# Kernel tuning notes

Hardware: AMD Instinct MI355X
Metric: run time of the kernel (lower is better)

The kernel has to match this reference:

```python
import jax, jax.numpy as jnp
import numpy as np

H = 256    # hidden_size
CVQ = 64   # vq_ph_channel
K = 128    # vq_ph_codebook_dim
NL = 5     # num_layers per ConvBlocks
NB = 2     # layers_in_block
KS = 3     # kernel_size


def _ln_c(x, g, b, eps=1e-5):
    # LayerNorm over channel dim of a [B, C, T] tensor
    m = jnp.mean(x, axis=1, keepdims=True)
    v = jnp.mean((x - m) ** 2, axis=1, keepdims=True)
    return (x - m) * jax.lax.rsqrt(v + eps) * g[None, :, None] + b[None, :, None]


def _causal_conv(x, w, b):
    # x [B,Cin,T], w [Cout,Cin,K]; left (causal) padding of K-1
    y = jax.lax.conv_general_dilated(x, w, (1,), [(w.shape[-1] - 1, 0)],
                                     dimension_numbers=('NCH', 'OIH', 'NCH'))
    return y + b[None, :, None]


def _pw(x, w, b):
    # pointwise (kernel-size-1) conv: w [Cout, Cin]
    return jnp.einsum('oi,bit->bot', w, x) + b[None, :, None]


def _conv_blocks(x, mask, ln_g, ln_b, w1, b1, w2, b2, last_g, last_b, post_w, post_b):
    # LeftPadConvBlocks: NL residual blocks x NB sub-blocks of
    # LN -> causal conv (C->2C, k=3) -> *k^-0.5 -> GELU -> 1x1 conv (2C->C), residual + mask
    scale = KS ** -0.5
    for i in range(NL):
        for j in range(NB):
            h = _ln_c(x, ln_g[i, j], ln_b[i, j])
            h = _causal_conv(h, w1[i, j], b1[i, j]) * scale
            h = jax.nn.gelu(h, approximate=False)
            h = _pw(h, w2[i, j], b2[i, j])
            x = (x + h) * mask
    x = _ln_c(x, last_g, last_b) * mask
    x = _causal_conv(x, post_w, post_b) * mask
    return x


def _group_by_segs(h_bct, mel2ph, L):
    # scatter-mean mel frames into phoneme segments; index 0 = padding (dropped)
    h = jnp.swapaxes(h_bct, 1, 2)  # [B, T, H]
    def one(hb, mb):
        s = jnp.zeros((L + 1, hb.shape[-1]), hb.dtype).at[mb].add(hb)
        c = jnp.zeros((L + 1,), hb.dtype).at[mb].add(1.0)
        return s[1:] / jnp.clip(c[1:], 1.0)[:, None]
    g = jax.vmap(one)(h, mel2ph)   # [B, L, H]
    return jnp.swapaxes(g, 1, 2)   # [B, H, L]


def _vq(z, codebook, beta=0.25):
    # EMA-VQ forward math: nearest-codebook lookup + straight-through + commitment loss
    x = jnp.swapaxes(z, 1, 2)                                # [B, T, C]
    d = (jnp.sum(x ** 2, -1, keepdims=True)
         - 2.0 * jnp.einsum('btc,kc->btk', x, codebook)
         + jnp.sum(codebook ** 2, -1))                       # [B, T, K]
    idx = jnp.argmin(d, axis=-1)                             # [B, T]
    q = codebook[idx]                                        # [B, T, C]
    loss = beta * jnp.mean((x - jax.lax.stop_gradient(q)) ** 2)
    q_st = x + jax.lax.stop_gradient(q - x)
    return jnp.swapaxes(q_st, 1, 2), loss, idx


def setup_inputs() -> dict:
    key = jax.random.key(0)
    ks = list(jax.random.split(key, 64))
    it = iter(ks)
    B, T, L = 16, 2048, 512
    f = lambda shape, s: jax.random.normal(next(it), shape, jnp.float32) * s
    inp = {}
    inp['x'] = jax.random.normal(next(it), (B, 80, T), jnp.float32)
    inp['in_nonpadding'] = jnp.ones((B, 1, T), jnp.float32)
    inp['in_mel2ph'] = jnp.sort(jax.random.randint(next(it), (B, T), 1, L + 1), axis=-1)
    inp['ph_nonpadding'] = jnp.ones((B, 1, L), jnp.float32)
    inp['conv_in_w'] = f((H, 80), 0.05)
    inp['conv_in_b'] = jnp.zeros((H,), jnp.float32)
    for p in ('enc', 'pn'):
        inp[p + '_ln_g'] = jnp.ones((NL, NB, H), jnp.float32)
        inp[p + '_ln_b'] = jnp.zeros((NL, NB, H), jnp.float32)
        inp[p + '_w1'] = f((NL, NB, 2 * H, H, KS), 0.03)
        inp[p + '_b1'] = jnp.zeros((NL, NB, 2 * H), jnp.float32)
        inp[p + '_w2'] = f((NL, NB, H, 2 * H), 0.03)
        inp[p + '_b2'] = jnp.zeros((NL, NB, H), jnp.float32)
        inp[p + '_last_g'] = jnp.ones((H,), jnp.float32)
        inp[p + '_last_b'] = jnp.zeros((H,), jnp.float32)
        inp[p + '_post_w'] = f((H, H, KS), 0.03)
        inp[p + '_post_b'] = jnp.zeros((H,), jnp.float32)
    inp['proj_in_w'] = f((CVQ, H), 0.05)
    inp['proj_in_b'] = jnp.zeros((CVQ,), jnp.float32)
    inp['proj_out_w'] = f((H, CVQ), 0.05)
    inp['proj_out_b'] = jnp.zeros((H,), jnp.float32)
    inp['codebook'] = f((K, CVQ), 0.1)
    return inp


def reference(x, in_nonpadding, in_mel2ph, ph_nonpadding,
              conv_in_w, conv_in_b,
              enc_ln_g, enc_ln_b, enc_w1, enc_b1, enc_w2, enc_b2,
              enc_last_g, enc_last_b, enc_post_w, enc_post_b,
              pn_ln_g, pn_ln_b, pn_w1, pn_b1, pn_w2, pn_b2,
              pn_last_g, pn_last_b, pn_post_w, pn_post_b,
              proj_in_w, proj_in_b, proj_out_w, proj_out_b, codebook):
    L = ph_nonpadding.shape[-1]
    h = _pw(x, conv_in_w, conv_in_b) * in_nonpadding                     # ph_conv_in
    h = _conv_blocks(h, in_nonpadding, enc_ln_g, enc_ln_b, enc_w1, enc_b1,
                     enc_w2, enc_b2, enc_last_g, enc_last_b,
                     enc_post_w, enc_post_b) * in_nonpadding             # ph_encoder
    h = _group_by_segs(h, in_mel2ph, L)                                  # [B, H, L]
    h = _conv_blocks(h, ph_nonpadding, pn_ln_g, pn_ln_b, pn_w1, pn_b1,
                     pn_w2, pn_b2, pn_last_g, pn_last_b,
                     pn_post_w, pn_post_b) * ph_nonpadding               # ph_postnet
    z = _pw(h, proj_in_w, proj_in_b)                                     # ph_latents_proj_in
    q, vq_loss, idx = _vq(z, codebook)                                   # VQ
    out = _pw(q, proj_out_w, proj_out_b)                                 # ph_latents_proj_out
    return out, vq_loss, idx
```

## Files before the change

kernel.cpp:

```cpp
#include <hip/hip_runtime.h>
#include <hip/hip_bf16.h>


typedef unsigned short u16;
typedef unsigned int u32;
typedef __attribute__((ext_vector_type(8))) _Float16 f16x8;
typedef __attribute__((ext_vector_type(16))) float f32x16;

#define OUT_LOSS_OFF 2097152
#define OUT_IDX_OFF  2097153

__device__ __forceinline__ void split_f16(float x, u16& h, u16& l) {
    union { _Float16 f; u16 u; } a, b;
    a.f = (_Float16)x;
    float hf = (float)a.f;
    b.f = (_Float16)(x - hf);
    h = a.u; l = b.u;
}

__device__ __forceinline__ void gelu_pack(float v, float bb, u16* GH, u16* GL,
                                          int off) {
    const float ks = 0.5773502691896258f;
    float y = (v + bb) * ks;
    float ge = 0.5f * y * (1.0f + erff(y * 0.7071067811865476f));
    u16 h, l; split_f16(ge, h, l);
    GH[off] = h; GL[off] = l;
}

__global__ __launch_bounds__(256) void k_t_mat(const float* __restrict__ w,
                                               float* __restrict__ wt,
                                               int G, int O, int I) {
    size_t n = (size_t)G * O * I;
    for (size_t i = (size_t)blockIdx.x * 256 + threadIdx.x; i < n;
         i += (size_t)gridDim.x * 256) {
        int ci = (int)(i % I);
        int o  = (int)((i / I) % O);
        int g  = (int)(i / ((size_t)I * O));
        wt[((size_t)g * I + ci) * O + o] = w[i];
    }
}

__global__ __launch_bounds__(256) void k_t_w1mf(const float* __restrict__ w,
                                                u16* __restrict__ BH,
                                                u16* __restrict__ BL, int S) {
    size_t N = (size_t)S * 3 * 16 * 16 * 64 * 8;
    for (size_t i = (size_t)blockIdx.x * 256 + threadIdx.x; i < N;
         i += (size_t)gridDim.x * 256) {
        int j = (int)(i & 7); size_t r = i >> 3;
        int L = (int)(r & 63); r >>= 6;
        int nt = (int)(r & 15); r >>= 4;
        int kb = (int)(r & 15); r >>= 4;
        int k3 = (int)(r % 3); int s = (int)(r / 3);
        int oc = nt * 32 + (L & 31);
        int c = kb * 16 + ((L >> 5) << 3) + j;
        float v = w[(((size_t)s * 512 + oc) * 256 + c) * 3 + k3];
        u16 h, l; split_f16(v, h, l);
        BH[i] = h; BL[i] = l;
    }
}

__global__ __launch_bounds__(256) void k_t_w2mf(const float* __restrict__ w,
                                                u16* __restrict__ BH,
                                                u16* __restrict__ BL, int S) {
    size_t N = (size_t)S * 32 * 8 * 64 * 8;
    for (size_t i = (size_t)blockIdx.x * 256 + threadIdx.x; i < N;
         i += (size_t)gridDim.x * 256) {
        int j = (int)(i & 7);
        int L = (int)((i >> 3) & 63);
        int nt = (int)((i >> 9) & 7);
        int kb = (int)((i >> 12) & 31);
        int s = (int)(i >> 17);
        int oc = nt * 32 + (L & 31);
        int ic = kb * 16 + ((L >> 5) << 3) + j;
        float v = w[((size_t)s * 256 + oc) * 512 + ic];
        u16 h, l; split_f16(v, h, l);
        BH[i] = h; BL[i] = l;
    }
}

__global__ __launch_bounds__(256) void k_t_wpmf(const float* __restrict__ w,
                                                u16* __restrict__ BH,
                                                u16* __restrict__ BL) {
    int i = blockIdx.x * 256 + threadIdx.x;
    int j = i & 7;
    int L = (i >> 3) & 63;
    int nt = (i >> 9) & 7;
    int kb = (i >> 12) & 15;
    int k3 = i >> 16;
    int oc = nt * 32 + (L & 31);
    int c = kb * 16 + ((L >> 5) << 3) + j;
    float v = w[((size_t)oc * 256 + c) * 3 + k3];
    u16 h, l; split_f16(v, h, l);
    BH[i] = h; BL[i] = l;
}

template <int CIN, int COUT, int CHUNK, bool STATS>
__global__ __launch_bounds__(256) void k_pw(const float* __restrict__ x,
                                            const float* __restrict__ wt,
                                            const float* __restrict__ bias,
                                            const float* __restrict__ mask,
                                            float* __restrict__ y,
                                            float* __restrict__ MM,
                                            float* __restrict__ IV, int T) {
    extern __shared__ float X[];
    constexpr int NG = COUT / CHUNK;
    __shared__ float rs[64 * NG], rs2[64 * NG];
    const int b = blockIdx.y, t0 = blockIdx.x * 64;
    for (int i = threadIdx.x; i < CIN * 64; i += 256) {
        int ci = i >> 6, j = i & 63;
        X[i] = x[((size_t)b * CIN + ci) * T + t0 + j];
    }
    __syncthreads();
    const int tl = threadIdx.x & 63;
    const int g = __builtin_amdgcn_readfirstlane((int)(threadIdx.x >> 6));
    float acc[CHUNK];
#pragma unroll
    for (int o = 0; o < CHUNK; o++) acc[o] = 0.f;
    for (int i = 0; i < CIN; i++) {
        float xv = X[i * 64 + tl];
        const float* wr = wt + (size_t)i * COUT + g * CHUNK;
#pragma unroll
        for (int o = 0; o < CHUNK; o++) acc[o] = fmaf(wr[o], xv, acc[o]);
    }
    float mk = mask ? mask[(size_t)b * T + t0 + tl] : 1.0f;
    float s = 0.f, s2 = 0.f;
#pragma unroll
    for (int o = 0; o < CHUNK; o++) {
        int oc = g * CHUNK + o;
        float val = (acc[o] + bias[oc]) * mk;
        y[((size_t)b * COUT + oc) * T + t0 + tl] = val;
        s += val; s2 += val * val;
    }
    if constexpr (STATS) {
        rs[g * 64 + tl] = s; rs2[g * 64 + tl] = s2;
        __syncthreads();
        if (threadIdx.x < 64) {
            float ss = 0.f, ss2 = 0.f;
#pragma unroll
            for (int gg = 0; gg < NG; gg++) {
                ss += rs[gg * 64 + threadIdx.x];
                ss2 += rs2[gg * 64 + threadIdx.x];
            }
            float m = ss * (1.0f / COUT);
            float var = ss2 * (1.0f / COUT) - m * m;
            MM[(size_t)b * T + t0 + threadIdx.x] = m;
            IV[(size_t)b * T + t0 + threadIdx.x] = 1.0f / sqrtf(var + 1e-5f);
        }
    }
}

template <int M>
__global__ __launch_bounds__(512, 4) void k_sub(
    const float* __restrict__ xin, float* __restrict__ xout,
    const float* __restrict__ MMi, const float* __restrict__ IVi,
    const float* __restrict__ lng, const float* __restrict__ lnb,
    const u16* __restrict__ B1H, const u16* __restrict__ B1L,
    const float* __restrict__ b1,
    const u16* __restrict__ B2H, const u16* __restrict__ B2L,
    const float* __restrict__ b2, const float* __restrict__ mask,
    float* __restrict__ MMo, float* __restrict__ IVo, int T) {
    constexpr int MT = M / 32;
    constexpr int SH = (M + 2) * 264 * 2;
    constexpr int CG = 512 / M;
    constexpr int CPT = 256 / CG;
    __shared__ __align__(16) char smem[2 * SH + 4096];
    u16* LH = (u16*)smem;
    u16* LL = (u16*)(smem + SH);
    u16* GH = (u16*)smem;
    u16* GL = (u16*)(smem + SH);
    float* SOUT = (float*)smem;
    float* rs  = (float*)(smem + 2 * SH);
    float* rs2 = (float*)(smem + 2 * SH + 2048);

    const int tid = threadIdx.x;
    const int b = blockIdx.y, t0 = blockIdx.x * M;
    const size_t xoff = (size_t)b * 256 * T;
    const size_t bT = (size_t)b * T;

    {
        int jj = tid & (M - 1);
        int cg = tid / M;
        int t = t0 - 2 + jj;
        bool ok = (t >= 0);
        float m = ok ? MMi[bT + t] : 0.f;
        float v = ok ? IVi[bT + t] : 0.f;
#pragma unroll
        for (int i = 0; i < CPT; i++) {
            int c = cg + i * CG;
            float xv = ok ? xin[xoff + (size_t)c * T + t] : 0.f;
            float ln = ok ? ((xv - m) * v * lng[c] + lnb[c]) : 0.f;
            u16 h, l; split_f16(ln, h, l);
            LH[jj * 264 + c] = h; LL[jj * 264 + c] = l;
        }
        int j2 = M + (tid >> 8);
        int c2 = tid & 255;
        int t2 = t0 + (M - 2) + (tid >> 8);
        float m2 = MMi[bT + t2], v2 = IVi[bT + t2];
        float x2 = xin[xoff + (size_t)c2 * T + t2];
        float ln2 = (x2 - m2) * v2 * lng[c2] + lnb[c2];
        u16 h2, l2; split_f16(ln2, h2, l2);
        LH[j2 * 264 + c2] = h2; LL[j2 * 264 + c2] = l2;
    }
    __syncthreads();

    const int lane = tid & 63;
    const int w = tid >> 6;
    const int arow = lane & 31;
    const int acol = (lane >> 5) << 3;
    const int thalf = (lane >> 5) << 2;
    const int oc_l = w * 32 + (lane & 31);
    const u16* b1h0 = B1H + (size_t)w * 512 + (size_t)lane * 8;
    const u16* b1l0 = B1L + (size_t)w * 512 + (size_t)lane * 8;
    const u16* b1h1 = B1H + (size_t)(8 + w) * 512 + (size_t)lane * 8;
    const u16* b1l1 = B1L + (size_t)(8 + w) * 512 + (size_t)lane * 8;
    const u16* b2h = B2H + (size_t)w * 512 + (size_t)lane * 8;
    const u16* b2l = B2L + (size_t)w * 512 + (size_t)lane * 8;

    f32x16 c0[MT], c1[MT];
#pragma unroll
    for (int m = 0; m < MT; m++)
#pragma unroll
        for (int r = 0; r < 16; r++) { c0[m][r] = 0.f; c1[m][r] = 0.f; }
    __builtin_amdgcn_s_setprio(1);
#pragma unroll 2
    for (int kk = 0; kk < 48; kk++) {
        int k3 = kk >> 4, kb = kk & 15;
        f16x8 bh0 = *(const f16x8*)(b1h0 + (size_t)kk * 8192);
        f16x8 bl0 = *(const f16x8*)(b1l0 + (size_t)kk * 8192);
        f16x8 bh1 = *(const f16x8*)(b1h1 + (size_t)kk * 8192);
        f16x8 bl1 = *(const f16x8*)(b1l1 + (size_t)kk * 8192);
#pragma unroll
        for (int m = 0; m < MT; m++) {
            int ao = (m * 32 + arow + k3) * 264 + kb * 16 + acol;
            f16x8 ah = *(const f16x8*)&LH[ao];
            f16x8 al = *(const f16x8*)&LL[ao];
            c0[m] = __builtin_amdgcn_mfma_f32_32x32x16_f16(ah, bh0, c0[m], 0, 0, 0);
            c1[m] = __builtin_amdgcn_mfma_f32_32x32x16_f16(ah, bh1, c1[m], 0, 0, 0);
            c0[m] = __builtin_amdgcn_mfma_f32_32x32x16_f16(ah, bl0, c0[m], 0, 0, 0);
            c1[m] = __builtin_amdgcn_mfma_f32_32x32x16_f16(ah, bl1, c1[m], 0, 0, 0);
            c0[m] = __builtin_amdgcn_mfma_f32_32x32x16_f16(al, bh0, c0[m], 0, 0, 0);
            c1[m] = __builtin_amdgcn_mfma_f32_32x32x16_f16(al, bh1, c1[m], 0, 0, 0);
        }
    }
    __builtin_amdgcn_s_setprio(0);
    __syncthreads();

    {
        float bb = b1[oc_l];
#pragma unroll
        for (int m = 0; m < MT; m++)
#pragma unroll
            for (int r = 0; r < 16; r++) {
                int trow = m * 32 + thalf + ((r >> 2) << 3) + (r & 3);
                gelu_pack(c0[m][r], bb, GH, GL, trow * 264 + oc_l);
            }
    }
    __syncthreads();

#pragma unroll
    for (int m = 0; m < MT; m++)
#pragma unroll
        for (int r = 0; r < 16; r++) c0[m][r] = 0.f;
    __builtin_amdgcn_s_setprio(1);
#pragma unroll 2
    for (int i = 0; i < 16; i++) {
        f16x8 bh2 = *(const f16x8*)(b2h + (size_t)i * 4096);
        f16x8 bl2 = *(const f16x8*)(b2l + (size_t)i * 4096);
#pragma unroll
        for (int m = 0; m < MT; m++) {
            int go = (m * 32 + arow) * 264 + i * 16 + acol;
            f16x8 gh = *(const f16x8*)&GH[go];
            f16x8 gl = *(const f16x8*)&GL[go];
            c0[m] = __builtin_amdgcn_mfma_f32_32x32x16_f16(gh, bh2, c0[m], 0, 0, 0);
            c0[m] = __builtin_amdgcn_mfma_f32_32x32x16_f16(gh, bl2, c0[m], 0, 0, 0);
            c0[m] = __builtin_amdgcn_mfma_f32_32x32x16_f16(gl, bh2, c0[m], 0, 0, 0);
        }
    }
    __builtin_amdgcn_s_setprio(0);
    __syncthreads();

    {
        float bb = b1[256 + oc_l];
#pragma unroll
        for (int m = 0; m < MT; m++)
#pragma unroll
            for (int r = 0; r < 16; r++) {
                int trow = m * 32 + thalf + ((r >> 2) << 3) + (r & 3);
                gelu_pack(c1[m][r], bb, GH, GL, trow * 264 + oc_l);
            }
    }
    __syncthreads();

    __builtin_amdgcn_s_setprio(1);
#pragma unroll 2
    for (int i = 0; i < 16; i++) {
        f16x8 bh2 = *(const f16x8*)(b2h + (size_t)(16 + i) * 4096);
        f16x8 bl2 = *(const f16x8*)(b2l + (size_t)(16 + i) * 4096);
#pragma unroll
        for (int m = 0; m < MT; m++) {
            int go = (m * 32 + arow) * 264 + i * 16 + acol;
            f16x8 gh = *(const f16x8*)&GH[go];
            f16x8 gl = *(const f16x8*)&GL[go];
            c0[m] = __builtin_amdgcn_mfma_f32_32x32x16_f16(gh, bh2, c0[m], 0, 0, 0);
            c0[m] = __builtin_amdgcn_mfma_f32_32x32x16_f16(gh, bl2, c0[m], 0, 0, 0);
            c0[m] = __builtin_amdgcn_mfma_f32_32x32x16_f16(gl, bh2, c0[m], 0, 0, 0);
        }
    }
    __builtin_amdgcn_s_setprio(0);
    __syncthreads();

#pragma unroll
    for (int m = 0; m < MT; m++)
#pragma unroll
        for (int r = 0; r < 16; r++) {
            int trow = m * 32 + thalf + ((r >> 2) << 3) + (r & 3);
            SOUT[trow * 260 + oc_l] = c0[m][r];
        }
    __syncthreads();
    {
        int t = tid & (M - 1), cg = tid / M;
        float mk = mask[bT + t0 + t];
        float s = 0.f, s2 = 0.f;
#pragma unroll
        for (int i = 0; i < CPT; i++) {
            int c = cg * CPT + i;
            size_t adr = xoff + (size_t)c * T + t0 + t;
            float val = (xin[adr] + SOUT[t * 260 + c] + b2[c]) * mk;
            xout[adr] = val;
            s += val; s2 += val * val;
        }
        rs[tid] = s; rs2[tid] = s2;
    }
    __syncthreads();
    if (tid < M) {
        float ss = 0.f, ss2 = 0.f;
#pragma unroll
        for (int k = 0; k < CG; k++) {
            ss += rs[k * M + tid]; ss2 += rs2[k * M + tid];
        }
        float m = ss * (1.0f / 256.0f);
        float var = ss2 * (1.0f / 256.0f) - m * m;
        MMo[bT + t0 + tid] = m;
        IVo[bT + t0 + tid] = 1.0f / sqrtf(var + 1e-5f);
    }
}

__global__ __launch_bounds__(1024, 4) void k_sub16(
    const float* __restrict__ xin, float* __restrict__ xout,
    const float* __restrict__ MMi, const float* __restrict__ IVi,
    const float* __restrict__ lng, const float* __restrict__ lnb,
    const u16* __restrict__ B1H, const u16* __restrict__ B1L,
    const float* __restrict__ b1,
    const u16* __restrict__ B2H, const u16* __restrict__ B2L,
    const float* __restrict__ b2, const float* __restrict__ mask,
    float* __restrict__ MMo, float* __restrict__ IVo, int T) {
    __shared__ __align__(16) char smem[76800];
    u16* LH = (u16*)smem;
    u16* LL = (u16*)(smem + 17952);
    u16* GH = (u16*)smem;
    u16* GL = (u16*)(smem + 34304);
    float* SOUT = (float*)smem;
    float* rs  = (float*)(smem + 68608);
    float* rs2 = (float*)(smem + 72704);

    const int tid = threadIdx.x;
    const int b = blockIdx.y, t0 = blockIdx.x * 32;
    const size_t xoff = (size_t)b * 256 * T;
    const size_t bT = (size_t)b * T;

    {
        int jj = tid & 31;
        int cg = tid >> 5;
        int t = t0 - 2 + jj;
        bool ok = (t >= 0);
        float m = ok ? MMi[bT + t] : 0.f;
        float v = ok ? IVi[bT + t] : 0.f;
#pragma unroll
        for (int i = 0; i < 8; i++) {
            int c = cg + i * 32;
            float xv = ok ? xin[xoff + (size_t)c * T + t] : 0.f;
            float ln = ok ? ((xv - m) * v * lng[c] + lnb[c]) : 0.f;
            u16 h, l; split_f16(ln, h, l);
            LH[jj * 264 + c] = h; LL[jj * 264 + c] = l;
        }
        if (tid < 512) {
            int j2 = 32 + (tid >> 8);
            int c2 = tid & 255;
            int t2 = t0 + 30 + (tid >> 8);
            float ln2 = (xin[xoff + (size_t)c2 * T + t2] - MMi[bT + t2]) *
                        IVi[bT + t2] * lng[c2] + lnb[c2];
            u16 h2, l2; split_f16(ln2, h2, l2);
            LH[j2 * 264 + c2] = h2; LL[j2 * 264 + c2] = l2;
        }
    }
    __syncthreads();

    const int lane = tid & 63;
    const int w = tid >> 6;
    const int arow = lane & 31;
    const int acol = (lane >> 5) << 3;
    const int thalf = (lane >> 5) << 2;
    const int oc_l = w * 32 + (lane & 31);
    const u16* b1h = B1H + (size_t)w * 512 + (size_t)lane * 8;
    const u16* b1l = B1L + (size_t)w * 512 + (size_t)lane * 8;

    f32x16 cc;
#pragma unroll
    for (int r = 0; r < 16; r++) cc[r] = 0.f;
    __builtin_amdgcn_s_setprio(1);
#pragma unroll 4
    for (int kk = 0; kk < 48; kk++) {
        int k3 = kk >> 4, kb = kk & 15;
        int ao = (arow + k3) * 264 + kb * 16 + acol;
        f16x8 ah = *(const f16x8*)&LH[ao];
        f16x8 al = *(const f16x8*)&LL[ao];
        f16x8 bh = *(const f16x8*)(b1h + (size_t)kk * 8192);
        f16x8 bl = *(const f16x8*)(b1l + (size_t)kk * 8192);
        cc = __builtin_amdgcn_mfma_f32_32x32x16_f16(ah, bh, cc, 0, 0, 0);
        cc = __builtin_amdgcn_mfma_f32_32x32x16_f16(ah, bl, cc, 0, 0, 0);
        cc = __builtin_amdgcn_mfma_f32_32x32x16_f16(al, bh, cc, 0, 0, 0);
    }
    __builtin_amdgcn_s_setprio(0);
    __syncthreads();

    {
        float bb = b1[oc_l];
#pragma unroll
        for (int r = 0; r < 16; r++) {
            int trow = thalf + ((r >> 2) << 3) + (r & 3);
            gelu_pack(cc[r], bb, GH, GL, trow * 536 + oc_l);
        }
    }
    __syncthreads();

    const int nt2 = w & 7;
    const int ih = w >> 3;
    const u16* b2h = B2H + (size_t)nt2 * 512 + (size_t)lane * 8;
    const u16* b2l = B2L + (size_t)nt2 * 512 + (size_t)lane * 8;
#pragma unroll
    for (int r = 0; r < 16; r++) cc[r] = 0.f;
    __builtin_amdgcn_s_setprio(1);
#pragma unroll 4
    for (int i = 0; i < 16; i++) {
        int ii = ih * 16 + i;
        int go = arow * 536 + ii * 16 + acol;
        f16x8 gh = *(const f16x8*)&GH[go];
        f16x8 gl = *(const f16x8*)&GL[go];
        f16x8 bh2 = *(const f16x8*)(b2h + (size_t)ii * 4096);
        f16x8 bl2 = *(const f16x8*)(b2l + (size_t)ii * 4096);
        cc = __builtin_amdgcn_mfma_f32_32x32x16_f16(gh, bh2, cc, 0, 0, 0);
        cc = __builtin_amdgcn_mfma_f32_32x32x16_f16(gh, bl2, cc, 0, 0, 0);
        cc = __builtin_amdgcn_mfma_f32_32x32x16_f16(gl, bh2, cc, 0, 0, 0);
    }
    __builtin_amdgcn_s_setprio(0);
    __syncthreads();

    if (w < 8) {
#pragma unroll
        for (int r = 0; r < 16; r++) {
            int trow = thalf + ((r >> 2) << 3) + (r & 3);
            SOUT[trow * 260 + oc_l] = cc[r];
        }
    }
    __syncthreads();
    if (w >= 8) {
        int oc2 = nt2 * 32 + (lane & 31);
#pragma unroll
        for (int r = 0; r < 16; r++) {
            int trow = thalf + ((r >> 2) << 3) + (r & 3);
            SOUT[trow * 260 + oc2] += cc[r];
        }
    }
    __syncthreads();
    {
        int t = tid & 31, cg = tid >> 5;
        float mk = mask[bT + t0 + t];
        float s = 0.f, s2 = 0.f;
#pragma unroll
        for (int i = 0; i < 8; i++) {
            int c = cg * 8 + i;
            size_t adr = xoff + (size_t)c * T + t0 + t;
            float val = (xin[adr] + SOUT[t * 260 + c] + b2[c]) * mk;
            xout[adr] = val;
            s += val; s2 += val * val;
        }
        rs[tid] = s; rs2[tid] = s2;
    }
    __syncthreads();
    if (tid < 32) {
        float ss = 0.f, ss2 = 0.f;
#pragma unroll
        for (int k = 0; k < 32; k++) {
            ss += rs[k * 32 + tid]; ss2 += rs2[k * 32 + tid];
        }
        float m = ss * (1.0f / 256.0f);
        float var = ss2 * (1.0f / 256.0f) - m * m;
        MMo[bT + t0 + tid] = m;
        IVo[bT + t0 + tid] = 1.0f / sqrtf(var + 1e-5f);
    }
}

template <int M>
__global__ __launch_bounds__(512, (M == 32 ? 8 : 4)) void k_lnc(
    const float* __restrict__ xin, float* __restrict__ xout,
    const float* __restrict__ MM, const float* __restrict__ IV,
    const float* __restrict__ lg, const float* __restrict__ lb,
    const u16* __restrict__ BH, const u16* __restrict__ BL,
    const float* __restrict__ bias, const float* __restrict__ mask, int T) {
    constexpr int MT = M / 32;
    constexpr int SH = (M + 2) * 264 * 2;
    constexpr int CG = 512 / M;
    constexpr int CPT = 256 / CG;
    __shared__ __align__(16) char smem[2 * SH];
    u16* LH = (u16*)smem;
    u16* LL = (u16*)(smem + SH);
    float* SOUT = (float*)smem;

    const int tid = threadIdx.x;
    const int b = blockIdx.y, t0 = blockIdx.x * M;
    const size_t xoff = (size_t)b * 256 * T;
    const size_t bT = (size_t)b * T;

    {
        int jj = tid & (M - 1);
        int cg = tid / M;
        int t = t0 - 2 + jj;
        bool ok = (t >= 0);
        float m = ok ? MM[bT + t] : 0.f;
        float v = ok ? IV[bT + t] : 0.f;
        float mk = ok ? mask[bT + t] : 0.f;
#pragma unroll
        for (int i = 0; i < CPT; i++) {
            int c = cg + i * CG;
            float xv = ok ? xin[xoff + (size_t)c * T + t] : 0.f;
            float ln = ok ? ((xv - m) * v * lg[c] + lb[c]) * mk : 0.f;
            u16 h, l; split_f16(ln, h, l);
            LH[jj * 264 + c] = h; LL[jj * 264 + c] = l;
        }
        int j2 = M + (tid >> 8);
        int c2 = tid & 255;
        int t2 = t0 + (M - 2) + (tid >> 8);
        float ln2 = ((xin[xoff + (size_t)c2 * T + t2] - MM[bT + t2]) *
                     IV[bT + t2] * lg[c2] + lb[c2]) * mask[bT + t2];
        u16 h2, l2; split_f16(ln2, h2, l2);
        LH[j2 * 264 + c2] = h2; LL[j2 * 264 + c2] = l2;
    }
    __syncthreads();

    const int lane = tid & 63;
    const int w = tid >> 6;
    const int arow = lane & 31;
    const int acol = (lane >> 5) << 3;
    const int thalf = (lane >> 5) << 2;
    const u16* bph = BH + (size_t)w * 512 + (size_t)lane * 8;
    const u16* bpl = BL + (size_t)w * 512 + (size_t)lane * 8;

    f32x16 aH[MT], aM[MT];
#pragma unroll
    for (int m = 0; m < MT; m++)
#pragma unroll
        for (int r = 0; r < 16; r++) { aH[m][r] = 0.f; aM[m][r] = 0.f; }
    __builtin_amdgcn_s_setprio(1);
#pragma unroll 2
    for (int kk = 0; kk < 48; kk++) {
        int k3 = kk >> 4, kb = kk & 15;
        f16x8 bh = *(const f16x8*)(bph + (size_t)kk * 4096);
        f16x8 bl = *(const f16x8*)(bpl + (size_t)kk * 4096);
#pragma unroll
        for (int m = 0; m < MT; m++) {
            int ao = (m * 32 + arow + k3) * 264 + kb * 16 + acol;
            f16x8 ah = *(const f16x8*)&LH[ao];
            f16x8 al = *(const f16x8*)&LL[ao];
            aH[m] = __builtin_amdgcn_mfma_f32_32x32x16_f16(ah, bh, aH[m], 0, 0, 0);
            aM[m] = __builtin_amdgcn_mfma_f32_32x32x16_f16(ah, bl, aM[m], 0, 0, 0);
            aM[m] = __builtin_amdgcn_mfma_f32_32x32x16_f16(al, bh, aM[m], 0, 0, 0);
        }
    }
    __builtin_amdgcn_s_setprio(0);
    __syncthreads();
    {
        int oc = w * 32 + (lane & 31);
#pragma unroll
        for (int m = 0; m < MT; m++)
#pragma unroll
            for (int r = 0; r < 16; r++) {
                int trow = m * 32 + thalf + ((r >> 2) << 3) + (r & 3);
                SOUT[trow * 260 + oc] = aH[m][r] + aM[m][r];
            }
    }
    __syncthreads();
    {
        int t = tid & (M - 1), cg = tid / M;
        float mk = mask[bT + t0 + t];
#pragma unroll
        for (int i = 0; i < CPT; i++) {
            int c = cg * CPT + i;
            xout[xoff + (size_t)c * T + t0 + t] =
                (SOUT[t * 260 + c] + bias[c]) * mk;
        }
    }
}

__global__ __launch_bounds__(256) void k_counts(const int* __restrict__ m2p,
                                                int* __restrict__ cnt) {
    __shared__ int c[512];
    int b = blockIdx.x;
    for (int i = threadIdx.x; i < 512; i += 256) c[i] = 0;
    __syncthreads();
    for (int t = threadIdx.x; t < 2048; t += 256) {
        int p = m2p[b * 2048 + t];
        if (p >= 1 && p <= 512) atomicAdd(&c[p - 1], 1);
    }
    __syncthreads();
    for (int i = threadIdx.x; i < 512; i += 256) cnt[b * 512 + i] = c[i];
}

__global__ __launch_bounds__(256) void k_scatter(const float* __restrict__ h,
                                                 const int* __restrict__ m2p,
                                                 float* __restrict__ g) {
    extern __shared__ float sm[];
    float* HT = sm;
    int* ph = (int*)(sm + 256 * 65);
    int b = blockIdx.y, t0 = blockIdx.x * 64;
    if (threadIdx.x < 64) ph[threadIdx.x] = m2p[b * 2048 + t0 + threadIdx.x];
    for (int i = threadIdx.x; i < 256 * 64; i += 256) {
        int c = i >> 6, j = i & 63;
        HT[c * 65 + j] = h[((size_t)b * 256 + c) * 2048 + t0 + j];
    }
    __syncthreads();
    int c = threadIdx.x;
    float run = 0.f;
    int cur = ph[0];
    for (int j = 0; j < 64; j++) {
        int p = ph[j];
        if (p != cur) {
            if (cur >= 1 && cur <= 512)
                atomicAdd(&g[((size_t)b * 256 + c) * 512 + cur - 1], run);
            run = 0.f;
            cur = p;
        }
        run += HT[c * 65 + j];
    }
    if (cur >= 1 && cur <= 512)
        atomicAdd(&g[((size_t)b * 256 + c) * 512 + cur - 1], run);
}

__global__ __launch_bounds__(512) void k_postprep(float* __restrict__ g,
                                                  const int* __restrict__ cnt,
                                                  float* __restrict__ MM,
                                                  float* __restrict__ IV) {
    int b = blockIdx.x, l = threadIdx.x;
    int c1 = cnt[b * 512 + l];
    if (c1 < 1) c1 = 1;
    float rc = 1.0f / (float)c1;
    float s = 0.f, s2 = 0.f;
    for (int c = 0; c < 256; c++) {
        size_t idx = ((size_t)b * 256 + c) * 512 + l;
        float v = g[idx] * rc;
        g[idx] = v;
        s += v; s2 += v * v;
    }
    float m = s * (1.0f / 256.0f);
    float var = s2 * (1.0f / 256.0f) - m * m;
    MM[(size_t)b * 512 + l] = m;
    IV[(size_t)b * 512 + l] = 1.0f / sqrtf(var + 1e-5f);
}

__global__ __launch_bounds__(256) void k_vq(const float* __restrict__ z,
                                            const float* __restrict__ cb,
                                            int* __restrict__ idxout,
                                            float* __restrict__ out,
                                            float* __restrict__ lossacc) {
    int n = blockIdx.x * 256 + threadIdx.x;
    int b = n >> 9, l = n & 511;
    float zr[64];
#pragma unroll
    for (int c = 0; c < 64; c++) zr[c] = z[((size_t)b * 64 + c) * 512 + l];
    float best = 3.4e38f;
    int bi = 0;
    for (int k = 0; k < 128; k++) {
        const float* cr = cb + k * 64;
        float d = 0.f;
#pragma unroll
        for (int c = 0; c < 64; c++) {
            float t = zr[c] - cr[c];
            d = fmaf(t, t, d);
        }
        if (d < best) { best = d; bi = k; }
    }
    idxout[n] = bi;
    out[OUT_IDX_OFF + n] = (float)bi;
    atomicAdd(lossacc, best);
}

__global__ void k_loss(const float* __restrict__ acc, float* __restrict__ out) {
    if (threadIdx.x == 0 && blockIdx.x == 0)
        out[OUT_LOSS_OFF] = 0.25f * acc[0] * (1.0f / 524288.0f);
}

__global__ __launch_bounds__(256) void k_projout(const float* __restrict__ cb,
                                                 const int* __restrict__ idx,
                                                 const float* __restrict__ wt,
                                                 const float* __restrict__ bias,
                                                 float* __restrict__ out) {
    __shared__ float Q[64 * 64];
    __shared__ int ids[64];
    int b = blockIdx.y, l0 = blockIdx.x * 64;
    if (threadIdx.x < 64) ids[threadIdx.x] = idx[b * 512 + l0 + threadIdx.x];
    __syncthreads();
    for (int i = threadIdx.x; i < 4096; i += 256) {
        int c = i >> 6, l = i & 63;
        Q[c * 64 + l] = cb[ids[l] * 64 + c];
    }
    __syncthreads();
    int tl = threadIdx.x & 63;
    int g = __builtin_amdgcn_readfirstlane((int)(threadIdx.x >> 6));
    float acc[64];
#pragma unroll
    for (int o = 0; o < 64; o++) acc[o] = 0.f;
    for (int i = 0; i < 64; i++) {
        float xv = Q[i * 64 + tl];
        const float* wr = wt + i * 256 + g * 64;
#pragma unroll
        for (int o = 0; o < 64; o++) acc[o] = fmaf(wr[o], xv, acc[o]);
    }
#pragma unroll
    for (int o = 0; o < 64; o++) {
        int oc = g * 64 + o;
        out[(size_t)b * 131072 + (size_t)oc * 512 + l0 + tl] = acc[o] + bias[oc];
    }
}

extern "C" void kernel_launch(void* const* d_in, const int* in_sizes, int n_in,
                              void* d_out, int out_size, void* d_ws, size_t ws_size,
                              hipStream_t stream) {
    (void)in_sizes; (void)n_in; (void)out_size; (void)ws_size;
    const float* x          = (const float*)d_in[0];
    const float* in_np      = (const float*)d_in[1];
    const int*   mel2ph     = (const int*)d_in[2];
    const float* ph_np      = (const float*)d_in[3];
    const float* conv_in_w  = (const float*)d_in[4];
    const float* conv_in_b  = (const float*)d_in[5];
    const float* e_ln_g = (const float*)d_in[6];
    const float* e_ln_b = (const float*)d_in[7];
    const float* e_w1   = (const float*)d_in[8];
    const float* e_b1   = (const float*)d_in[9];
    const float* e_w2   = (const float*)d_in[10];
    const float* e_b2   = (const float*)d_in[11];
    const float* e_lg   = (const float*)d_in[12];
    const float* e_lb   = (const float*)d_in[13];
    const float* e_pw   = (const float*)d_in[14];
    const float* e_pb   = (const float*)d_in[15];
    const float* p_ln_g = (const float*)d_in[16];
    const float* p_ln_b = (const float*)d_in[17];
    const float* p_w1   = (const float*)d_in[18];
    const float* p_b1   = (const float*)d_in[19];
    const float* p_w2   = (const float*)d_in[20];
    const float* p_b2   = (const float*)d_in[21];
    const float* p_lg   = (const float*)d_in[22];
    const float* p_lb   = (const float*)d_in[23];
    const float* p_pw   = (const float*)d_in[24];
    const float* p_pb   = (const float*)d_in[25];
    const float* proj_in_w  = (const float*)d_in[26];
    const float* proj_in_b  = (const float*)d_in[27];
    const float* proj_out_w = (const float*)d_in[28];
    const float* proj_out_b = (const float*)d_in[29];
    const float* codebook   = (const float*)d_in[30];
    float* out = (float*)d_out;

    float* ws = (float*)d_ws;
    float* A      = ws;
    float* Bb     = A + 8388608;
    float* CINT   = Bb + 8388608;
    float* PINT   = CINT + 20480;
    float* POUTT  = PINT + 16384;
    float* Z      = POUTT + 16384;
    float* MM0    = Z + 524288;
    float* IV0    = MM0 + 32768;
    float* MM1    = IV0 + 32768;
    float* IV1    = MM1 + 32768;
    int*   CNT    = (int*)(IV1 + 32768);
    int*   IDX    = CNT + 8192;
    float* LOSS   = (float*)(IDX + 8192);
    u16*   BH1E   = (u16*)(LOSS + 64);
    u16*   BL1E   = BH1E + 3932160;
    u16*   BH1P   = BL1E + 3932160;
    u16*   BL1P   = BH1P + 3932160;
    u16*   BH2E   = BL1P + 3932160;
    u16*   BL2E   = BH2E + 1310720;
    u16*   BH2P   = BL2E + 1310720;
    u16*   BL2P   = BH2P + 1310720;
    u16*   PH_E   = BL2P + 1310720;
    u16*   PL_E   = PH_E + 196608;
    u16*   PH_P   = PL_E + 196608;
    u16*   PL_P   = PH_P + 196608;

    k_t_w1mf<<<dim3(4096), dim3(256), 0, stream>>>(e_w1, BH1E, BL1E, 10);
    k_t_w1mf<<<dim3(4096), dim3(256), 0, stream>>>(p_w1, BH1P, BL1P, 10);
    k_t_w2mf<<<dim3(2048), dim3(256), 0, stream>>>(e_w2, BH2E, BL2E, 10);
    k_t_w2mf<<<dim3(2048), dim3(256), 0, stream>>>(p_w2, BH2P, BL2P, 10);
    k_t_wpmf<<<dim3(768),  dim3(256), 0, stream>>>(e_pw, PH_E, PL_E);
    k_t_wpmf<<<dim3(768),  dim3(256), 0, stream>>>(p_pw, PH_P, PL_P);
    k_t_mat  <<<dim3(80),  dim3(256), 0, stream>>>(conv_in_w, CINT, 1, 256, 80);
    k_t_mat  <<<dim3(64),  dim3(256), 0, stream>>>(proj_in_w, PINT, 1, 64, 256);
    k_t_mat  <<<dim3(64),  dim3(256), 0, stream>>>(proj_out_w, POUTT, 1, 256, 64);

    const size_t sm_scat = 256 * 65 * sizeof(float) + 64 * sizeof(int);

    k_pw<80, 256, 64, true><<<dim3(32, 16), dim3(256), 80 * 64 * 4, stream>>>(
        x, CINT, conv_in_b, in_np, A, MM0, IV0, 2048);

    float* cur = A;
    float* nxt = Bb;
    for (int s = 0; s < 10; s++) {
        float* mi = (s & 1) ? MM1 : MM0;
        float* vi = (s & 1) ? IV1 : IV0;
        float* mo = (s & 1) ? MM0 : MM1;
        float* vo = (s & 1) ? IV0 : IV1;
        k_sub<64><<<dim3(32, 16), dim3(512), 0, stream>>>(
            cur, nxt, mi, vi, e_ln_g + s * 256, e_ln_b + s * 256,
            BH1E + (size_t)s * 393216, BL1E + (size_t)s * 393216, e_b1 + s * 512,
            BH2E + (size_t)s * 131072, BL2E + (size_t)s * 131072, e_b2 + s * 256,
            in_np, mo, vo, 2048);
        float* t = cur; cur = nxt; nxt = t;
    }
    k_lnc<64><<<dim3(32, 16), dim3(512), 0, stream>>>(
        cur, nxt, MM0, IV0, e_lg, e_lb, PH_E, PL_E, e_pb, in_np, 2048);

    hipMemsetAsync(A, 0, (size_t)2097152 * 4, stream);
    hipMemsetAsync(LOSS, 0, 4, stream);
    k_counts<<<dim3(16), dim3(256), 0, stream>>>(mel2ph, CNT);
    k_scatter<<<dim3(32, 16), dim3(256), sm_scat, stream>>>(Bb, mel2ph, A);
    k_postprep<<<dim3(16), dim3(512), 0, stream>>>(A, CNT, MM0, IV0);

    cur = A; nxt = Bb;
    for (int s = 0; s < 10; s++) {
        float* mi = (s & 1) ? MM1 : MM0;
        float* vi = (s & 1) ? IV1 : IV0;
        float* mo = (s & 1) ? MM0 : MM1;
        float* vo = (s & 1) ? IV0 : IV1;
        k_sub16<<<dim3(16, 16), dim3(1024), 0, stream>>>(
            cur, nxt, mi, vi, p_ln_g + s * 256, p_ln_b + s * 256,
            BH1P + (size_t)s * 393216, BL1P + (size_t)s * 393216, p_b1 + s * 512,
            BH2P + (size_t)s * 131072, BL2P + (size_t)s * 131072, p_b2 + s * 256,
            ph_np, mo, vo, 512);
        float* t = cur; cur = nxt; nxt = t;
    }
    k_lnc<32><<<dim3(16, 16), dim3(512), 0, stream>>>(
        cur, nxt, MM0, IV0, p_lg, p_lb, PH_P, PL_P, p_pb, ph_np, 512);

    k_pw<256, 64, 16, false><<<dim3(8, 16), dim3(256), 256 * 64 * 4, stream>>>(
        Bb, PINT, proj_in_b, nullptr, Z, nullptr, nullptr, 512);

    k_vq<<<dim3(32), dim3(256), 0, stream>>>(Z, codebook, IDX, out, LOSS);
    k_loss<<<dim3(1), dim3(64), 0, stream>>>(LOSS, out);
    k_projout<<<dim3(8, 16), dim3(256), 0, stream>>>(codebook, IDX, POUTT,
                                                     proj_out_b, out);
}
```

Before: 2.062 ms.

## Batch LDS loads before MFMA chains, split VQ search, drop extra sync

Result: no change. 2.061 ms (-0.1%).

```diff
diff --git a/kernel.cpp b/kernel.cpp
--- a/kernel.cpp
+++ b/kernel.cpp
@@ -229,17 +229,27 @@
         f16x8 bl0 = *(const f16x8*)(b1l0 + (size_t)kk * 8192);
         f16x8 bh1 = *(const f16x8*)(b1h1 + (size_t)kk * 8192);
         f16x8 bl1 = *(const f16x8*)(b1l1 + (size_t)kk * 8192);
+        f16x8 ah[MT], al[MT];
 #pragma unroll
         for (int m = 0; m < MT; m++) {
             int ao = (m * 32 + arow + k3) * 264 + kb * 16 + acol;
-            f16x8 ah = *(const f16x8*)&LH[ao];
-            f16x8 al = *(const f16x8*)&LL[ao];
-            c0[m] = __builtin_amdgcn_mfma_f32_32x32x16_f16(ah, bh0, c0[m], 0, 0, 0);
-            c1[m] = __builtin_amdgcn_mfma_f32_32x32x16_f16(ah, bh1, c1[m], 0, 0, 0);
-            c0[m] = __builtin_amdgcn_mfma_f32_32x32x16_f16(ah, bl0, c0[m], 0, 0, 0);
-            c1[m] = __builtin_amdgcn_mfma_f32_32x32x16_f16(ah, bl1, c1[m], 0, 0, 0);
-            c0[m] = __builtin_amdgcn_mfma_f32_32x32x16_f16(al, bh0, c0[m], 0, 0, 0);
-            c1[m] = __builtin_amdgcn_mfma_f32_32x32x16_f16(al, bh1, c1[m], 0, 0, 0);
+            ah[m] = *(const f16x8*)&LH[ao];
+            al[m] = *(const f16x8*)&LL[ao];
+        }
+#pragma unroll
+        for (int m = 0; m < MT; m++) {
+            c0[m] = __builtin_amdgcn_mfma_f32_32x32x16_f16(ah[m], bh0, c0[m], 0, 0, 0);
+            c1[m] = __builtin_amdgcn_mfma_f32_32x32x16_f16(ah[m], bh1, c1[m], 0, 0, 0);
+        }
+#pragma unroll
+        for (int m = 0; m < MT; m++) {
+            c0[m] = __builtin_amdgcn_mfma_f32_32x32x16_f16(ah[m], bl0, c0[m], 0, 0, 0);
+            c1[m] = __builtin_amdgcn_mfma_f32_32x32x16_f16(ah[m], bl1, c1[m], 0, 0, 0);
+        }
+#pragma unroll
+        for (int m = 0; m < MT; m++) {
+            c0[m] = __builtin_amdgcn_mfma_f32_32x32x16_f16(al[m], bh0, c0[m], 0, 0, 0);
+            c1[m] = __builtin_amdgcn_mfma_f32_32x32x16_f16(al[m], bh1, c1[m], 0, 0, 0);
         }
     }
     __builtin_amdgcn_s_setprio(0);
@@ -266,15 +276,22 @@
     for (int i = 0; i < 16; i++) {
         f16x8 bh2 = *(const f16x8*)(b2h + (size_t)i * 4096);
         f16x8 bl2 = *(const f16x8*)(b2l + (size_t)i * 4096);
+        f16x8 gh[MT], gl[MT];
 #pragma unroll
         for (int m = 0; m < MT; m++) {
             int go = (m * 32 + arow) * 264 + i * 16 + acol;
-            f16x8 gh = *(const f16x8*)&GH[go];
-            f16x8 gl = *(const f16x8*)&GL[go];
-            c0[m] = __builtin_amdgcn_mfma_f32_32x32x16_f16(gh, bh2, c0[m], 0, 0, 0);
-            c0[m] = __builtin_amdgcn_mfma_f32_32x32x16_f16(gh, bl2, c0[m], 0, 0, 0);
-            c0[m] = __builtin_amdgcn_mfma_f32_32x32x16_f16(gl, bh2, c0[m], 0, 0, 0);
-        }
+            gh[m] = *(const f16x8*)&GH[go];
+            gl[m] = *(const f16x8*)&GL[go];
+        }
+#pragma unroll
+        for (int m = 0; m < MT; m++)
+            c0[m] = __builtin_amdgcn_mfma_f32_32x32x16_f16(gh[m], bh2, c0[m], 0, 0, 0);
+#pragma unroll
+        for (int m = 0; m < MT; m++)
+            c0[m] = __builtin_amdgcn_mfma_f32_32x32x16_f16(gh[m], bl2, c0[m], 0, 0, 0);
+#pragma unroll
+        for (int m = 0; m < MT; m++)
+            c0[m] = __builtin_amdgcn_mfma_f32_32x32x16_f16(gl[m], bh2, c0[m], 0, 0, 0);
     }
     __builtin_amdgcn_s_setprio(0);
     __syncthreads();
@@ -296,15 +313,22 @@
     for (int i = 0; i < 16; i++) {
         f16x8 bh2 = *(const f16x8*)(b2h + (size_t)(16 + i) * 4096);
         f16x8 bl2 = *(const f16x8*)(b2l + (size_t)(16 + i) * 4096);
+        f16x8 gh[MT], gl[MT];
 #pragma unroll
         for (int m = 0; m < MT; m++) {
             int go = (m * 32 + arow) * 264 + i * 16 + acol;
-            f16x8 gh = *(const f16x8*)&GH[go];
-            f16x8 gl = *(const f16x8*)&GL[go];
-            c0[m] = __builtin_amdgcn_mfma_f32_32x32x16_f16(gh, bh2, c0[m], 0, 0, 0);
-            c0[m] = __builtin_amdgcn_mfma_f32_32x32x16_f16(gh, bl2, c0[m], 0, 0, 0);
-            c0[m] = __builtin_amdgcn_mfma_f32_32x32x16_f16(gl, bh2, c0[m], 0, 0, 0);
-        }
+            gh[m] = *(const f16x8*)&GH[go];
+            gl[m] = *(const f16x8*)&GL[go];
+        }
+#pragma unroll
+        for (int m = 0; m < MT; m++)
+            c0[m] = __builtin_amdgcn_mfma_f32_32x32x16_f16(gh[m], bh2, c0[m], 0, 0, 0);
+#pragma unroll
+        for (int m = 0; m < MT; m++)
+            c0[m] = __builtin_amdgcn_mfma_f32_32x32x16_f16(gh[m], bl2, c0[m], 0, 0, 0);
+#pragma unroll
+        for (int m = 0; m < MT; m++)
+            c0[m] = __builtin_amdgcn_mfma_f32_32x32x16_f16(gl[m], bh2, c0[m], 0, 0, 0);
     }
     __builtin_amdgcn_s_setprio(0);
     __syncthreads();
@@ -359,7 +383,8 @@
     u16* LL = (u16*)(smem + 17952);
     u16* GH = (u16*)smem;
     u16* GL = (u16*)(smem + 34304);
-    float* SOUT = (float*)smem;
+    float* SOUT  = (float*)smem;
+    float* SOUT2 = (float*)(smem + 34304);
     float* rs  = (float*)(smem + 68608);
     float* rs2 = (float*)(smem + 72704);
 
@@ -461,14 +486,12 @@
             int trow = thalf + ((r >> 2) << 3) + (r & 3);
             SOUT[trow * 260 + oc_l] = cc[r];
         }
-    }
-    __syncthreads();
-    if (w >= 8) {
+    } else {
         int oc2 = nt2 * 32 + (lane & 31);
 #pragma unroll
         for (int r = 0; r < 16; r++) {
             int trow = thalf + ((r >> 2) << 3) + (r & 3);
-            SOUT[trow * 260 + oc2] += cc[r];
+            SOUT2[trow * 260 + oc2] = cc[r];
         }
     }
     __syncthreads();
@@ -480,7 +503,8 @@
         for (int i = 0; i < 8; i++) {
             int c = cg * 8 + i;
             size_t adr = xoff + (size_t)c * T + t0 + t;
-            float val = (xin[adr] + SOUT[t * 260 + c] + b2[c]) * mk;
+            float val = (xin[adr] + (SOUT[t * 260 + c] + SOUT2[t * 260 + c]) +
+                         b2[c]) * mk;
             xout[adr] = val;
             s += val; s2 += val * val;
         }
@@ -566,15 +590,22 @@
         int k3 = kk >> 4, kb = kk & 15;
         f16x8 bh = *(const f16x8*)(bph + (size_t)kk * 4096);
         f16x8 bl = *(const f16x8*)(bpl + (size_t)kk * 4096);
+        f16x8 ah[MT], al[MT];
 #pragma unroll
         for (int m = 0; m < MT; m++) {
             int ao = (m * 32 + arow + k3) * 264 + kb * 16 + acol;
-            f16x8 ah = *(const f16x8*)&LH[ao];
-            f16x8 al = *(const f16x8*)&LL[ao];
-            aH[m] = __builtin_amdgcn_mfma_f32_32x32x16_f16(ah, bh, aH[m], 0, 0, 0);
-            aM[m] = __builtin_amdgcn_mfma_f32_32x32x16_f16(ah, bl, aM[m], 0, 0, 0);
-            aM[m] = __builtin_amdgcn_mfma_f32_32x32x16_f16(al, bh, aM[m], 0, 0, 0);
-        }
+            ah[m] = *(const f16x8*)&LH[ao];
+            al[m] = *(const f16x8*)&LL[ao];
+        }
+#pragma unroll
+        for (int m = 0; m < MT; m++)
+            aH[m] = __builtin_amdgcn_mfma_f32_32x32x16_f16(ah[m], bh, aH[m], 0, 0, 0);
+#pragma unroll
+        for (int m = 0; m < MT; m++)
+            aM[m] = __builtin_amdgcn_mfma_f32_32x32x16_f16(ah[m], bl, aM[m], 0, 0, 0);
+#pragma unroll
+        for (int m = 0; m < MT; m++)
+            aM[m] = __builtin_amdgcn_mfma_f32_32x32x16_f16(al[m], bh, aM[m], 0, 0, 0);
     }
     __builtin_amdgcn_s_setprio(0);
     __syncthreads();
@@ -671,14 +702,17 @@
                                             int* __restrict__ idxout,
                                             float* __restrict__ out,
                                             float* __restrict__ lossacc) {
-    int n = blockIdx.x * 256 + threadIdx.x;
+    int n2 = blockIdx.x * 256 + threadIdx.x;
+    int n = n2 >> 1;
+    int half = n2 & 1;
     int b = n >> 9, l = n & 511;
     float zr[64];
 #pragma unroll
     for (int c = 0; c < 64; c++) zr[c] = z[((size_t)b * 64 + c) * 512 + l];
     float best = 3.4e38f;
     int bi = 0;
-    for (int k = 0; k < 128; k++) {
+    int k0 = half * 64;
+    for (int k = k0; k < k0 + 64; k++) {
         const float* cr = cb + k * 64;
         float d = 0.f;
 #pragma unroll
@@ -688,9 +722,14 @@
         }
         if (d < best) { best = d; bi = k; }
     }
-    idxout[n] = bi;
-    out[OUT_IDX_OFF + n] = (float)bi;
-    atomicAdd(lossacc, best);
+    float bestO = __shfl_xor(best, 1);
+    int biO = __shfl_xor(bi, 1);
+    if (bestO < best || (bestO == best && biO < bi)) { best = bestO; bi = biO; }
+    if (half == 0) {
+        idxout[n] = bi;
+        out[OUT_IDX_OFF + n] = (float)bi;
+        atomicAdd(lossacc, best);
+    }
 }
 
 __global__ void k_loss(const float* __restrict__ acc, float* __restrict__ out) {
@@ -852,7 +891,7 @@
     k_pw<256, 64, 16, false><<<dim3(8, 16), dim3(256), 256 * 64 * 4, stream>>>(
         Bb, PINT, proj_in_b, nullptr, Z, nullptr, nullptr, 512);
 
-    k_vq<<<dim3(32), dim3(256), 0, stream>>>(Z, codebook, IDX, out, LOSS);
+    k_vq<<<dim3(64), dim3(256), 0, stream>>>(Z, codebook, IDX, out, LOSS);
     k_loss<<<dim3(1), dim3(64), 0, stream>>>(LOSS, out);
     k_projout<<<dim3(8, 16), dim3(256), 0, stream>>>(codebook, IDX, POUTT,
                                                      proj_out_b, out);
```
